# Optimization experiments

Hardware: AMD Instinct MI355X
Metric: run time of the kernel (lower is better)

The kernel has to match this reference:

```python
import jax, jax.numpy as jnp
import numpy as np

K = 3          # kernel_size
STRIDE = 1
PAD = 1
BASIS = 8      # act_fun.get_size() (Hermite basis order)


def _unfold(x):
    # x: [B, Cin, H, W] -> patches [B, Cin, K*K, L] (same ordering as F.unfold)
    b, c, h, w = x.shape
    p = jax.lax.conv_general_dilated_patches(
        x, filter_shape=(K, K), window_strides=(STRIDE, STRIDE),
        padding=[(PAD, PAD), (PAD, PAD)])
    # p: [B, Cin*K*K, Hout, Wout], channel-major ordering (Cin, Kh, Kw)
    ho, wo = p.shape[2], p.shape[3]
    return p.reshape(b, c, K * K, ho * wo), ho, wo


def _hermite(x):
    # Physicists' Hermite polynomials H_0..H_{BASIS-1}, stacked on last axis.
    hs = [jnp.ones_like(x), 2.0 * x]
    for n in range(1, BASIS - 1):
        hs.append(2.0 * x * hs[n] - 2.0 * n * hs[n - 1])
    return jnp.stack(hs[:BASIS], axis=-1)


def setup_inputs() -> dict:
    key = jax.random.key(0)
    k1, k2, k3, k4 = jax.random.split(key, 4)
    cin, cout = 64, 128
    x = jax.random.normal(k1, (16, cin, 32, 32), dtype=jnp.float32)
    # xavier_normal on [Cin,Cout,K^2,1]: std = sqrt(2/(fan_in+fan_out)) over last two dims -> use small randn
    w_b = jax.random.normal(k2, (cin, cout, K * K, 1), dtype=jnp.float32)
    w_s = jax.random.normal(k3, (cin, cout, K * K, 1), dtype=jnp.float32) * 0.001
    c = jax.random.normal(k4, (cin, cout, K * K, 1, BASIS), dtype=jnp.float32) * 0.1
    return {"x": x, "w_b": w_b, "w_s": w_s, "c": c}


def reference(x, w_b, w_s, c):
    b = x.shape[0]
    xw, ho, wo = _unfold(x)                      # [B, Cin, K2, L]
    phi = _hermite(xw)                           # [B, Cin, K2, L, BASIS]
    res = jax.nn.silu(xw)                        # residual activation
    # effective spline weight: w_s * c, contracted over Cin, K2, basis
    cw = w_s[..., 0, None] * c[:, :, :, 0, :]    # [Cin, Cout, K2, BASIS]
    out = (jnp.einsum('ioka,bikla->bol', cw, phi)
           + jnp.einsum('iok,bikl->bol', w_b[..., 0], res))  # [B, Cout, L]
    return out.reshape(b, -1, ho, wo)
```

## Files before the change

kernel.cpp:

```cpp
#include <hip/hip_runtime.h>
#include <stdint.h>

typedef unsigned short ushort_t;
typedef short short8 __attribute__((ext_vector_type(8)));
typedef float f32x4 __attribute__((ext_vector_type(4)));

#define CIN   64
#define COUT  128
#define BATCH 16
#define LPIX  1024
#define NTOT  (BATCH*LPIX)
#define C2N   576
#define PIXN  (BATCH*34*34)
#define NSTEP2 72
#define KS    4
#define PART_ELEMS (NTOT*COUT)
#define FEAT_BLOCKS (PIXN/4)
#define WPREP_BLOCKS (COUT*NSTEP2*64/256)

#define FEAT_BYTES (PIXN*C2N*2)
#define W_OFF      FEAT_BYTES
#define W_BYTES    (COUT*NSTEP2*64*2)
#define BIAS_OFF   (W_OFF + W_BYTES)
#define PART_OFF   (BIAS_OFF + 512)
#define PART_BYTES (PART_ELEMS*4)
#define WS_NEED    ((size_t)PART_OFF + (size_t)(KS-1)*PART_BYTES)

#define WAITVM(n) asm volatile("s_waitcnt vmcnt(" #n ")" ::: "memory")
#define BAR() __builtin_amdgcn_s_barrier()

__device__ __forceinline__ ushort_t to_bf16(float f) {
  union { float f; uint32_t u; } v; v.f = f;
  uint32_t r = (v.u + 0x7fffu + ((v.u >> 16) & 1u)) >> 16;
  return (ushort_t)r;
}

__device__ __forceinline__ void basis9(float x, float* o) {
  float hm = 1.f, h = 2.f * x;
  o[0] = hm; o[1] = h;
#pragma unroll
  for (int n = 1; n < 7; ++n) {
    float nx = 2.f * x * h - 2.f * (float)n * hm;
    hm = h; h = nx;
    o[n + 1] = nx;
  }
  o[8] = x / (1.f + __expf(-x));
}

__device__ __forceinline__ void load16(const void* g, void* l) {
  __builtin_amdgcn_global_load_lds(
      (const __attribute__((address_space(1))) uint32_t*)g,
      (__attribute__((address_space(3))) uint32_t*)l, 16, 0, 0);
}

__global__ void prep_kernel(const float* __restrict__ x, ushort_t* __restrict__ feat,
                            const float* __restrict__ wb, const float* __restrict__ wsp,
                            const float* __restrict__ cc, ushort_t* __restrict__ W,
                            float* __restrict__ bias) {
  __shared__ float red[4];
  const int t = threadIdx.x;
  if (blockIdx.x < FEAT_BLOCKS) {
    const int lane = t & 63;
    const int pg = blockIdx.x * 4 + (t >> 6);
    const int xx = pg % 34;
    const int rest = pg / 34;
    const int yy = rest % 34;
    const int bb = rest / 34;
    float v = 0.f;
    if (xx >= 1 && xx <= 32 && yy >= 1 && yy <= 32)
      v = x[((bb * CIN + lane) * 32 + (yy - 1)) * 32 + (xx - 1)];
    float o[9];
    basis9(v, o);
    ushort_t* dst = feat + (size_t)pg * C2N + lane;
#pragma unroll
    for (int f = 1; f < 9; ++f) dst[f * 64] = to_bf16(o[f]);
  } else if (blockIdx.x < FEAT_BLOCKS + WPREP_BLOCKS) {
    const int idx = (blockIdx.x - FEAT_BLOCKS) * 256 + t;
    const int m = idx / (NSTEP2 * 64);
    const int pos = idx - m * (NSTEP2 * 64);
    const int s = pos >> 6;
    const int r = pos & 63;
    const int i = ((((r >> 3) & 7) ^ (m & 7)) << 3) | (r & 7);
    const int sf = 1 + s / 9;
    const int kk = s % 9;
    const int base = (i * COUT + m) * 9 + kk;
    const float val = (sf < 8) ? wsp[base] * cc[base * 8 + sf] : wb[base];
    W[idx] = to_bf16(val);
  } else {
    const int m = blockIdx.x - (FEAT_BLOCKS + WPREP_BLOCKS);
    float p = 0.f;
    for (int e = t; e < CIN * 9; e += 256) {
      const int i = e / 9, kk = e - i * 9;
      const int base = (i * COUT + m) * 9 + kk;
      p += wsp[base] * cc[base * 8];
    }
#pragma unroll
    for (int off = 32; off > 0; off >>= 1) p += __shfl_down(p, off, 64);
    if ((t & 63) == 0) red[t >> 6] = p;
    __syncthreads();
    if (t == 0) bias[m] = red[0] + red[1] + red[2] + red[3];
  }
}

__global__ __launch_bounds__(256, 2) void gemm_kernel(const ushort_t* __restrict__ feat,
                                                      const ushort_t* __restrict__ W,
                                                      const float* __restrict__ bias,
                                                      float* __restrict__ out,
                                                      float* __restrict__ part) {
  __shared__ ushort_t Ab[4][4096];
  __shared__ ushort_t Hb[2720 * 8];
  const int t = threadIdx.x;
  const int lane = t & 63;
  const int wn = t >> 6;

  const int logical = (blockIdx.x & 7) * 64 + (blockIdx.x >> 3);
  const int nb = logical >> 3;
  const int rem = logical & 7;
  const int mt = rem >> 2;
  const int ksplit = rem & 3;
  const int lo = ksplit * 18;

  const int b  = nb >> 2;
  const int y0 = (nb & 3) * 8;
  const int pixbase = (b * 34 + y0) * 34;

  const char* Wb = (const char*)W + mt * 64 * (NSTEP2 * 64 * 2);
  const char* Fb = (const char*)feat;

  f32x4 acc[4][4];
#pragma unroll
  for (int a = 0; a < 4; ++a)
#pragma unroll
    for (int c = 0; c < 4; ++c) acc[a][c] = (f32x4)0.f;

  auto stage_halo = [&](int c2s) {
    const char* base = Fb + (size_t)pixbase * (C2N * 2) + (c2s + 1) * 128;
#pragma unroll
    for (int it = 0; it < 11; ++it) {
      const int q = it * 256 + t;
      if (q < 2720) {
        const int L = q >> 3;
        const int sl = (q & 7) ^ (L & 7);
        load16(base + L * (C2N * 2) + (sl << 4), &Hb[q * 8]);
      }
    }
  };

  auto stageA = [&](int p, int s) {
#pragma unroll
    for (int q = 0; q < 2; ++q) {
      const int idx16 = q * 256 + t;
      const int m = idx16 >> 3, ccn = idx16 & 7;
      load16(Wb + m * (NSTEP2 * 64 * 2) + s * 128 + ccn * 16, &Ab[p][idx16 * 8]);
    }
  };

  auto compute = [&](int p, int j) {
    const int dy = j / 3, dx = j - dy * 3;
#pragma unroll
    for (int ks = 0; ks < 2; ++ks) {
      short8 av[4], bv[4];
      const int kslot = ks * 4 + (lane >> 4);
#pragma unroll
      for (int mf = 0; mf < 4; ++mf) {
        const int row = mf * 16 + (lane & 15);
        av[mf] = *(const short8*)&Ab[p][row * 64 + ((kslot ^ (row & 7)) << 3)];
      }
#pragma unroll
      for (int nf = 0; nf < 4; ++nf) {
        const int nl = wn * 64 + nf * 16 + (lane & 15);
        const int L = ((nl >> 5) + dy) * 34 + (nl & 31) + dx;
        bv[nf] = *(const short8*)&Hb[L * 64 + ((kslot ^ (L & 7)) << 3)];
      }
#pragma unroll
      for (int mf = 0; mf < 4; ++mf)
#pragma unroll
        for (int nf = 0; nf < 4; ++nf)
          acc[mf][nf] = __builtin_amdgcn_mfma_f32_16x16x32_bf16(av[mf], bv[nf],
                                                                acc[mf][nf], 0, 0, 0);
    }
  };

#define GSTEP(j, N)                                         \
  {                                                         \
    if ((j) + 2 < 18) stageA(((j) + 2) & 3, lo + (j) + 2);  \
    WAITVM(N);                                              \
    BAR();                                                  \
    compute((j) & 3, (j) % 9);                              \
  }

  stage_halo(2 * ksplit);
  stageA(0, lo);
  stageA(1, lo + 1);

  GSTEP(0, 4);  GSTEP(1, 4);  GSTEP(2, 4);  GSTEP(3, 4);  GSTEP(4, 4);
  GSTEP(5, 4);  GSTEP(6, 4);  GSTEP(7, 4);  GSTEP(8, 4);

  BAR();
  stage_halo(2 * ksplit + 1);

  GSTEP(9, 2);  GSTEP(10, 4); GSTEP(11, 4); GSTEP(12, 4); GSTEP(13, 4);
  GSTEP(14, 4); GSTEP(15, 4); GSTEP(16, 2); GSTEP(17, 0);
#undef GSTEP

  float* dst = ksplit ? (part + (size_t)(ksplit - 1) * PART_ELEMS) : out;
#pragma unroll
  for (int mf = 0; mf < 4; ++mf)
#pragma unroll
    for (int rg = 0; rg < 4; ++rg) {
      const int m = mt * 64 + mf * 16 + (lane >> 4) * 4 + rg;
      const float bv = ksplit ? 0.f : bias[m];
#pragma unroll
      for (int nf = 0; nf < 4; ++nf) {
        const int n = nb * 256 + wn * 64 + nf * 16 + (lane & 15);
        const int bb = n >> 10, ll = n & 1023;
        dst[(bb * COUT + m) * LPIX + ll] = acc[mf][nf][rg] + bv;
      }
    }
}

template <int NP>
__global__ void add_kernel(float* __restrict__ out, const float* __restrict__ part) {
  const int i = (blockIdx.x * 256 + threadIdx.x) * 4;
  f32x4 a = *(const f32x4*)&out[i];
#pragma unroll
  for (int j = 0; j < NP; ++j)
    a += *(const f32x4*)&part[(size_t)j * PART_ELEMS + i];
  *(f32x4*)&out[i] = a;
}

__global__ void naive_kernel(const float* __restrict__ x, const float* __restrict__ wb,
                             const float* __restrict__ wsp, const float* __restrict__ cc,
                             float* __restrict__ out) {
  const int idx = blockIdx.x * 256 + threadIdx.x;
  if (idx >= BATCH * COUT * LPIX) return;
  const int l = idx & 1023, o = (idx >> 10) & 127, b = idx >> 17;
  const int h = l >> 5, w = l & 31;
  float acc = 0.f;
  for (int i = 0; i < CIN; ++i)
    for (int kk = 0; kk < 9; ++kk) {
      const int yy = h + kk / 3 - 1, xx = w + kk % 3 - 1;
      const float v = (yy >= 0 && yy < 32 && xx >= 0 && xx < 32)
                          ? x[((b * CIN + i) * 32 + yy) * 32 + xx] : 0.f;
      float ftr[9];
      basis9(v, ftr);
      const int base = (i * COUT + o) * 9 + kk;
      const float* cp = cc + base * 8;
      float dot = 0.f;
#pragma unroll
      for (int f = 0; f < 8; ++f) dot += cp[f] * ftr[f];
      acc += wsp[base] * dot + wb[base] * ftr[8];
    }
  out[idx] = acc;
}

extern "C" void kernel_launch(void* const* d_in, const int* in_sizes, int n_in,
                              void* d_out, int out_size, void* d_ws, size_t ws_size,
                              hipStream_t stream) {
  const float* x  = (const float*)d_in[0];
  const float* wb = (const float*)d_in[1];
  const float* wsp = (const float*)d_in[2];
  const float* cc = (const float*)d_in[3];
  float* out = (float*)d_out;

  if (ws_size < WS_NEED) {
    naive_kernel<<<(BATCH * COUT * LPIX + 255) / 256, 256, 0, stream>>>(x, wb, wsp, cc, out);
    return;
  }

  char* ws = (char*)d_ws;
  ushort_t* feat = (ushort_t*)ws;
  ushort_t* W    = (ushort_t*)(ws + W_OFF);
  float* bias    = (float*)(ws + BIAS_OFF);
  float* part    = (float*)(ws + PART_OFF);

  prep_kernel<<<FEAT_BLOCKS + WPREP_BLOCKS + COUT, 256, 0, stream>>>(x, feat, wb, wsp, cc, W, bias);
  gemm_kernel<<<64 * 2 * KS, 256, 0, stream>>>(feat, W, bias, out, part);
  add_kernel<KS - 1><<<PART_ELEMS / 1024, 256, 0, stream>>>(out, part);
}
```

Baseline: 45.88 us.

## Store split-K partials in bf16, restructure weight prep, raise MFMA priority

The split-K partial sums are now written and read as bf16 instead of fp32, which halves the partial-buffer traffic between the GEMM and the reduction kernel. The reduction kernel now handles 8 elements per thread. Weight preparation is restructured: each block computes 4 output rows through an LDS staging buffer, coalesces the cc reads, and folds the bias reduction into the same blocks. This cuts the prep block count. The MFMA loop is wrapped in s_setprio raises. Rounding partial sums to bf16 adds precision loss to the output.

```diff
diff --git a/kernel.cpp b/kernel.cpp
--- a/kernel.cpp
+++ b/kernel.cpp
@@ -16,14 +16,14 @@
 #define KS    4
 #define PART_ELEMS (NTOT*COUT)
 #define FEAT_BLOCKS (PIXN/4)
-#define WPREP_BLOCKS (COUT*NSTEP2*64/256)
+#define WPREP_BLOCKS 32
 
 #define FEAT_BYTES (PIXN*C2N*2)
 #define W_OFF      FEAT_BYTES
 #define W_BYTES    (COUT*NSTEP2*64*2)
 #define BIAS_OFF   (W_OFF + W_BYTES)
 #define PART_OFF   (BIAS_OFF + 512)
-#define PART_BYTES (PART_ELEMS*4)
+#define PART_BYTES (PART_ELEMS*2)
 #define WS_NEED    ((size_t)PART_OFF + (size_t)(KS-1)*PART_BYTES)
 
 #define WAITVM(n) asm volatile("s_waitcnt vmcnt(" #n ")" ::: "memory")
@@ -34,6 +34,10 @@
   uint32_t r = (v.u + 0x7fffu + ((v.u >> 16) & 1u)) >> 16;
   return (ushort_t)r;
 }
+__device__ __forceinline__ float from_bf16(ushort_t u) {
+  union { uint32_t u; float f; } v; v.u = ((uint32_t)u) << 16;
+  return v.f;
+}
 
 __device__ __forceinline__ void basis9(float x, float* o) {
   float hm = 1.f, h = 2.f * x;
@@ -57,7 +61,8 @@
                             const float* __restrict__ wb, const float* __restrict__ wsp,
                             const float* __restrict__ cc, ushort_t* __restrict__ W,
                             float* __restrict__ bias) {
-  __shared__ float red[4];
+  __shared__ ushort_t wl[4][NSTEP2 * 64 + 16];
+  __shared__ float bl[16];
   const int t = threadIdx.x;
   if (blockIdx.x < FEAT_BLOCKS) {
     const int lane = t & 63;
@@ -74,31 +79,39 @@
     ushort_t* dst = feat + (size_t)pg * C2N + lane;
 #pragma unroll
     for (int f = 1; f < 9; ++f) dst[f * 64] = to_bf16(o[f]);
-  } else if (blockIdx.x < FEAT_BLOCKS + WPREP_BLOCKS) {
-    const int idx = (blockIdx.x - FEAT_BLOCKS) * 256 + t;
-    const int m = idx / (NSTEP2 * 64);
-    const int pos = idx - m * (NSTEP2 * 64);
-    const int s = pos >> 6;
-    const int r = pos & 63;
-    const int i = ((((r >> 3) & 7) ^ (m & 7)) << 3) | (r & 7);
-    const int sf = 1 + s / 9;
-    const int kk = s % 9;
-    const int base = (i * COUT + m) * 9 + kk;
-    const float val = (sf < 8) ? wsp[base] * cc[base * 8 + sf] : wb[base];
-    W[idx] = to_bf16(val);
   } else {
-    const int m = blockIdx.x - (FEAT_BLOCKS + WPREP_BLOCKS);
-    float p = 0.f;
-    for (int e = t; e < CIN * 9; e += 256) {
-      const int i = e / 9, kk = e - i * 9;
-      const int base = (i * COUT + m) * 9 + kk;
-      p += wsp[base] * cc[base * 8];
-    }
-#pragma unroll
-    for (int off = 32; off > 0; off >>= 1) p += __shfl_down(p, off, 64);
-    if ((t & 63) == 0) red[t >> 6] = p;
+    const int mg = blockIdx.x - FEAT_BLOCKS;
+    const int i = t >> 2;
+    const int mq = t & 3;
+    const int m = mg * 4 + mq;
+    const int base = (i * COUT + m) * 9;
+    const int r = ((((i >> 3) & 7) ^ (m & 7)) << 3) | (i & 7);
+    float h0 = 0.f;
+#pragma unroll
+    for (int kk = 0; kk < 9; ++kk) {
+      const float ws_ = wsp[base + kk];
+      const float wbv = wb[base + kk];
+      const float* cp = cc + (size_t)(base + kk) * 8;
+      h0 += ws_ * cp[0];
+#pragma unroll
+      for (int sf = 1; sf <= 8; ++sf) {
+        const float val = (sf < 8) ? ws_ * cp[sf] : wbv;
+        wl[mq][((sf - 1) * 9 + kk) * 64 + r] = to_bf16(val);
+      }
+    }
+#pragma unroll
+    for (int off = 4; off < 64; off <<= 1) h0 += __shfl_down(h0, off, 64);
+    if ((t & 63) < 4) bl[(t >> 6) * 4 + (t & 3)] = h0;
     __syncthreads();
-    if (t == 0) bias[m] = red[0] + red[1] + red[2] + red[3];
+    if (t < 4) bias[mg * 4 + t] = bl[t] + bl[4 + t] + bl[8 + t] + bl[12 + t];
+#pragma unroll 4
+    for (int jj = 0; jj < 36; ++jj) {
+      const int flat = jj * 256 + t;
+      const int row = flat >> 5, col = flat & 31;
+      const int mq2 = row / NSTEP2, s2 = row - mq2 * NSTEP2;
+      const uint32_t v = *(const uint32_t*)&wl[mq2][s2 * 64 + col * 2];
+      *(uint32_t*)&W[(size_t)(mg * 4 + mq2) * (NSTEP2 * 64) + s2 * 64 + col * 2] = v;
+    }
   }
 }
 
@@ -106,7 +119,7 @@
                                                       const ushort_t* __restrict__ W,
                                                       const float* __restrict__ bias,
                                                       float* __restrict__ out,
-                                                      float* __restrict__ part) {
+                                                      ushort_t* __restrict__ part) {
   __shared__ ushort_t Ab[4][4096];
   __shared__ ushort_t Hb[2720 * 8];
   const int t = threadIdx.x;
@@ -172,12 +185,14 @@
         const int L = ((nl >> 5) + dy) * 34 + (nl & 31) + dx;
         bv[nf] = *(const short8*)&Hb[L * 64 + ((kslot ^ (L & 7)) << 3)];
       }
+      __builtin_amdgcn_s_setprio(1);
 #pragma unroll
       for (int mf = 0; mf < 4; ++mf)
 #pragma unroll
         for (int nf = 0; nf < 4; ++nf)
           acc[mf][nf] = __builtin_amdgcn_mfma_f32_16x16x32_bf16(av[mf], bv[nf],
                                                                 acc[mf][nf], 0, 0, 0);
+      __builtin_amdgcn_s_setprio(0);
     }
   };
 
@@ -203,30 +218,52 @@
   GSTEP(14, 4); GSTEP(15, 4); GSTEP(16, 2); GSTEP(17, 0);
 #undef GSTEP
 
-  float* dst = ksplit ? (part + (size_t)(ksplit - 1) * PART_ELEMS) : out;
-#pragma unroll
-  for (int mf = 0; mf < 4; ++mf)
-#pragma unroll
-    for (int rg = 0; rg < 4; ++rg) {
-      const int m = mt * 64 + mf * 16 + (lane >> 4) * 4 + rg;
-      const float bv = ksplit ? 0.f : bias[m];
-#pragma unroll
-      for (int nf = 0; nf < 4; ++nf) {
-        const int n = nb * 256 + wn * 64 + nf * 16 + (lane & 15);
-        const int bb = n >> 10, ll = n & 1023;
-        dst[(bb * COUT + m) * LPIX + ll] = acc[mf][nf][rg] + bv;
-      }
-    }
-}
-
-template <int NP>
-__global__ void add_kernel(float* __restrict__ out, const float* __restrict__ part) {
-  const int i = (blockIdx.x * 256 + threadIdx.x) * 4;
-  f32x4 a = *(const f32x4*)&out[i];
-#pragma unroll
-  for (int j = 0; j < NP; ++j)
-    a += *(const f32x4*)&part[(size_t)j * PART_ELEMS + i];
-  *(f32x4*)&out[i] = a;
+  if (ksplit) {
+    ushort_t* dst = part + (size_t)(ksplit - 1) * PART_ELEMS;
+#pragma unroll
+    for (int mf = 0; mf < 4; ++mf)
+#pragma unroll
+      for (int rg = 0; rg < 4; ++rg) {
+        const int m = mt * 64 + mf * 16 + (lane >> 4) * 4 + rg;
+#pragma unroll
+        for (int nf = 0; nf < 4; ++nf) {
+          const int n = nb * 256 + wn * 64 + nf * 16 + (lane & 15);
+          const int bb = n >> 10, ll = n & 1023;
+          dst[(bb * COUT + m) * LPIX + ll] = to_bf16(acc[mf][nf][rg]);
+        }
+      }
+  } else {
+#pragma unroll
+    for (int mf = 0; mf < 4; ++mf)
+#pragma unroll
+      for (int rg = 0; rg < 4; ++rg) {
+        const int m = mt * 64 + mf * 16 + (lane >> 4) * 4 + rg;
+        const float bv = bias[m];
+#pragma unroll
+        for (int nf = 0; nf < 4; ++nf) {
+          const int n = nb * 256 + wn * 64 + nf * 16 + (lane & 15);
+          const int bb = n >> 10, ll = n & 1023;
+          out[(bb * COUT + m) * LPIX + ll] = acc[mf][nf][rg] + bv;
+        }
+      }
+  }
+}
+
+__global__ void add_kernel(float* __restrict__ out, const ushort_t* __restrict__ part) {
+  const int i = (blockIdx.x * 256 + threadIdx.x) * 8;
+  f32x4 a0 = *(const f32x4*)&out[i];
+  f32x4 a1 = *(const f32x4*)&out[i + 4];
+#pragma unroll
+  for (int j = 0; j < KS - 1; ++j) {
+    const short8 pv = *(const short8*)&part[(size_t)j * PART_ELEMS + i];
+#pragma unroll
+    for (int e = 0; e < 4; ++e) {
+      a0[e] += from_bf16((ushort_t)pv[e]);
+      a1[e] += from_bf16((ushort_t)pv[e + 4]);
+    }
+  }
+  *(f32x4*)&out[i] = a0;
+  *(f32x4*)&out[i + 4] = a1;
 }
 
 __global__ void naive_kernel(const float* __restrict__ x, const float* __restrict__ wb,
@@ -272,9 +309,9 @@
   ushort_t* feat = (ushort_t*)ws;
   ushort_t* W    = (ushort_t*)(ws + W_OFF);
   float* bias    = (float*)(ws + BIAS_OFF);
-  float* part    = (float*)(ws + PART_OFF);
-
-  prep_kernel<<<FEAT_BLOCKS + WPREP_BLOCKS + COUT, 256, 0, stream>>>(x, feat, wb, wsp, cc, W, bias);
+  ushort_t* part = (ushort_t*)(ws + PART_OFF);
+
+  prep_kernel<<<FEAT_BLOCKS + WPREP_BLOCKS, 256, 0, stream>>>(x, feat, wb, wsp, cc, W, bias);
   gemm_kernel<<<64 * 2 * KS, 256, 0, stream>>>(feat, W, bias, out, part);
-  add_kernel<KS - 1><<<PART_ELEMS / 1024, 256, 0, stream>>>(out, part);
-}
+  add_kernel<<<PART_ELEMS / 2048, 256, 0, stream>>>(out, part);
+}
```

After: 45.55 us. Within noise of the previous version (-0.7%).
